# Kernel tuning notes

Measured on AMD Instinct MI355X. Metric: run time of the kernel, lower is better.

## Reference

```python
import jax, jax.numpy as jnp
import numpy as np

M = 16           # size_graph_filter (nodes per hidden prototype graph)
S = 16           # size_subgraph
D_IN = 128       # input_dim
H = 64           # hidden_dim
O = 32           # out_dim (number of hidden prototype graphs)
B = 32768        # batch of subgraphs
MAX_STEP = 3
BN_EPS = 1e-5


def setup_inputs() -> dict:
    key = jax.random.key(0)
    ks = jax.random.split(key, 8)
    adj = jax.random.uniform(ks[0], (B, S, S), dtype=jnp.float32)
    adj = 0.5 * (adj + jnp.swapaxes(adj, 1, 2))  # symmetric weighted adjacency
    features = jax.random.normal(ks[1], (B, S, D_IN), dtype=jnp.float32)
    # learned parameters (per torch init: uniform inits, Linear default-like fc_in)
    W_in = jax.random.normal(ks[2], (D_IN, H), dtype=jnp.float32) * (1.0 / np.sqrt(D_IN))
    b_in = jnp.zeros((H,), dtype=jnp.float32)
    features_hidden = jax.random.uniform(ks[3], (M, H, O), dtype=jnp.float32)          # U(0,1)
    adj_hidden = jax.random.uniform(ks[4], (M * (M - 1) // 2, O), dtype=jnp.float32,
                                    minval=-1.0, maxval=1.0)                            # U(-1,1)
    bn_gamma = jnp.ones((O,), dtype=jnp.float32)
    bn_beta = jnp.zeros((O,), dtype=jnp.float32)
    return {"adj": adj, "features": features, "W_in": W_in, "b_in": b_in,
            "features_hidden": features_hidden, "adj_hidden": adj_hidden,
            "bn_gamma": bn_gamma, "bn_beta": bn_beta}


def reference(adj, features, W_in, b_in, features_hidden, adj_hidden, bn_gamma, bn_beta):
    # Build symmetric hidden adjacency (M, M, O) from triu-packed parameters.
    iu, ju = jnp.triu_indices(M, k=1)
    A = jnp.zeros((M, M, O), dtype=adj_hidden.dtype)
    A = A.at[iu, ju, :].set(jax.nn.relu(adj_hidden))
    A = A + jnp.swapaxes(A, 0, 1)

    x = jax.nn.sigmoid(features @ W_in + b_in)   # (B, S, H)
    z = features_hidden                           # (M, H, O)

    acc = jnp.zeros((B, O), dtype=x.dtype)
    for step in range(MAX_STEP):
        if step > 0:
            x = jnp.einsum('bst,bth->bsh', adj, x)        # propagate on input subgraphs
            z = jnp.einsum('mpo,pho->mho', A, z)          # propagate on hidden graphs
        # random-walk kernel value between each subgraph and each prototype
        t = jnp.einsum('mho,bsh->bo', z, x)               # sum over prototype & subgraph nodes
        acc = acc + t
    out = acc / MAX_STEP

    # BatchNorm1d (training-mode batch statistics), then sigmoid; dropout p used in eval = identity
    mean = jnp.mean(out, axis=0)
    var = jnp.var(out, axis=0)
    out = (out - mean) / jnp.sqrt(var + BN_EPS) * bn_gamma + bn_beta
    return jax.nn.sigmoid(out)
```

## Files before the change

kernel.cpp:

```cpp
#include <hip/hip_runtime.h>


typedef short  vec8s  __attribute__((ext_vector_type(8)));
typedef short  vec4s  __attribute__((ext_vector_type(4)));
typedef float  f32x4  __attribute__((ext_vector_type(4)));
typedef unsigned short vec4us __attribute__((ext_vector_type(4)));

#define NB      32768
#define SS      16
#define DIN     128
#define HH      64
#define OO      32
#define MM      16

__device__ __forceinline__ float bf2f(unsigned short u) {
    return __uint_as_float(((unsigned int)u) << 16);
}
__device__ __forceinline__ unsigned short f2bf(float f) {
    unsigned int u = __float_as_uint(f);
    unsigned int r = (u + 0x7fffu + ((u >> 16) & 1u)) >> 16;
    return (unsigned short)r;
}
template<bool F32>
__device__ __forceinline__ float ldv(const void* p, int i) {
    if (F32) return ((const float*)p)[i];
    return bf2f(((const unsigned short*)p)[i]);
}
__device__ __forceinline__ vec8s pack8(f32x4 lo, f32x4 hi) {
    union { unsigned int u[4]; vec8s v; } r;
    unsigned int a0 = __float_as_uint(lo[0]) + 0x8000u;
    unsigned int a1 = __float_as_uint(lo[1]) + 0x8000u;
    unsigned int a2 = __float_as_uint(lo[2]) + 0x8000u;
    unsigned int a3 = __float_as_uint(lo[3]) + 0x8000u;
    unsigned int b0 = __float_as_uint(hi[0]) + 0x8000u;
    unsigned int b1 = __float_as_uint(hi[1]) + 0x8000u;
    unsigned int b2 = __float_as_uint(hi[2]) + 0x8000u;
    unsigned int b3 = __float_as_uint(hi[3]) + 0x8000u;
    r.u[0] = (a0 >> 16) | (a1 & 0xFFFF0000u);
    r.u[1] = (a2 >> 16) | (a3 & 0xFFFF0000u);
    r.u[2] = (b0 >> 16) | (b1 & 0xFFFF0000u);
    r.u[3] = (b2 >> 16) | (b3 & 0xFFFF0000u);
    return r.v;
}

template<bool F32>
__device__ __forceinline__ float Aval(const void* ahS, int i, int j, int o) {
    if (i == j) return 0.f;
    int a = i < j ? i : j;
    int b = i < j ? j : i;
    int idx = a * 15 - ((a * (a - 1)) >> 1) + (b - a - 1);
    float v = ldv<F32>(ahS, idx * OO + o);
    return v > 0.f ? v : 0.f;
}

template<bool F32>
__device__ void k1_body(const void* fhP, const void* ahP, const void* WP,
                        short* ZcnS, short* WtS, float* cA, float* c2) {
    const int tid = threadIdx.x;
    for (int i = tid; i < MM * OO; i += 256) {
        int p = i >> 5, o = i & 31;
        float s = 0.f;
        for (int m = 0; m < MM; ++m) s += Aval<F32>(ahP, m, p, o);
        cA[i] = s;
    }
    __syncthreads();
    for (int i = tid; i < MM * OO; i += 256) {
        int qq = i >> 5, o = i & 31;
        float s = 0.f;
        for (int p = 0; p < MM; ++p) s += cA[p * OO + o] * Aval<F32>(ahP, p, qq, o);
        c2[i] = s;
    }
    __syncthreads();
    for (int i = blockIdx.x * 256 + tid; i < 3 * OO * HH; i += 16 * 256) {
        int n = i >> 6, h = i & 63;
        int step = n >> 5, o = n & 31;
        float v = 0.f;
        for (int p = 0; p < MM; ++p) {
            float z = ldv<F32>(fhP, p * (HH * OO) + h * OO + o);
            float w = (step == 0) ? 1.f : (step == 1 ? cA[p * OO + o] : c2[p * OO + o]);
            v += w * z;
        }
        ZcnS[n * HH + h] = (short)f2bf(v);
    }
    for (int i = blockIdx.x * 256 + tid; i < DIN * HH; i += 16 * 256) {
        int h = i >> 7, k = i & 127;
        WtS[h * DIN + k] = (short)f2bf(ldv<F32>(WP, k * HH + h));
    }
}

__global__ void k1_prep(const void* fhP, const void* ahP, const void* WP,
                        short* ZcnS, short* WtS, double* dstats,
                        const void* featP, int* flag) {
    __shared__ float cA[MM * OO];
    __shared__ float c2[MM * OO];
    __shared__ int chuge, czero, sflag;
    const int tid = threadIdx.x;
    if (tid == 0) { chuge = 0; czero = 0; }
    if (blockIdx.x == 0 && tid < 64) dstats[tid] = 0.0;
    __syncthreads();
    if (tid < 64) {
        const unsigned short* p = (const unsigned short*)featP;
        int h = 0, z = 0;
        for (int i = tid; i < 4096; i += 64) {
            unsigned short u = p[i];
            unsigned e = (u >> 7) & 0xFFu;
            if (e >= 0x90u) h++;
            if ((u & 0x7FFFu) == 0) z++;
        }
        atomicAdd(&chuge, h);
        atomicAdd(&czero, z);
    }
    __syncthreads();
    if (tid == 0) {
        sflag = (chuge > 8 || czero > 512) ? 1 : 0;
        if (blockIdx.x == 0) *flag = sflag;
    }
    __syncthreads();
    if (sflag) k1_body<true>(fhP, ahP, WP, ZcnS, WtS, cA, c2);
    else       k1_body<false>(fhP, ahP, WP, ZcnS, WtS, cA, c2);
}


template<bool F32> struct Slot;
template<> struct Slot<true>  { f32x4 f[8]; f32x4 a; };
template<> struct Slot<false> { vec8s f[4]; vec4s a; };

template<bool F32>
__device__ __forceinline__ void issue_load(const void* adjP, const void* featP,
                                           int b, int lane, int hl, int q,
                                           Slot<F32>& s) {
    if constexpr (F32) {
        s.a = *(const f32x4*)((const float*)adjP + b * (SS * SS) + lane * 4);
        const float* fb = (const float*)featP + b * (SS * DIN) + hl * DIN + q * 8;
        #pragma unroll
        for (int kt = 0; kt < 4; ++kt) {
            s.f[2 * kt]     = *(const f32x4*)(fb + kt * 32);
            s.f[2 * kt + 1] = *(const f32x4*)(fb + kt * 32 + 4);
        }
    } else {
        s.a = *(const vec4s*)((const short*)adjP + b * (SS * SS) + lane * 4);
        const short* fb = (const short*)featP + b * (SS * DIN) + hl * DIN + q * 8;
        #pragma unroll
        for (int kt = 0; kt < 4; ++kt) s.f[kt] = *(const vec8s*)(fb + kt * 32);
    }
}

template<bool F32>
__device__ __forceinline__ void compute_one(
    const Slot<F32>& s, int b,
    const vec8s (&Wfrag)[4][4], const char* ZcnL,
    const float (&biasv)[4], short* myx0, float* accOut,
    float& ls, float& lss, int lane, int hl, int q) {

    const f32x4 z4 = {0.f, 0.f, 0.f, 0.f};

    float a0, a1, a2, a3;
    vec8s af[4];
    if constexpr (F32) {
        a0 = s.a[0]; a1 = s.a[1]; a2 = s.a[2]; a3 = s.a[3];
        #pragma unroll
        for (int kt = 0; kt < 4; ++kt) af[kt] = pack8(s.f[2 * kt], s.f[2 * kt + 1]);
    } else {
        a0 = bf2f((unsigned short)s.a.x); a1 = bf2f((unsigned short)s.a.y);
        a2 = bf2f((unsigned short)s.a.z); a3 = bf2f((unsigned short)s.a.w);
        #pragma unroll
        for (int kt = 0; kt < 4; ++kt) af[kt] = s.f[kt];
    }

    float rsum = a0 + a1 + a2 + a3;
    rsum += __shfl_xor(rsum, 1);
    rsum += __shfl_xor(rsum, 2);
    int cg = lane & 3;
    float rr0 = __shfl(rsum, cg * 16 + 0);
    float rr1 = __shfl(rsum, cg * 16 + 4);
    float rr2 = __shfl(rsum, cg * 16 + 8);
    float rr3 = __shfl(rsum, cg * 16 + 12);
    float p = a0 * rr0 + a1 * rr1 + a2 * rr2 + a3 * rr3;
    p += __shfl_xor(p, 1);
    p += __shfl_xor(p, 2);
    float w1q[4], w2q[4];
    #pragma unroll
    for (int reg = 0; reg < 4; ++reg) {
        int src = q * 16 + reg * 4;
        w1q[reg] = __shfl(rsum, src);
        w2q[reg] = __shfl(p, src);
    }

    f32x4 c1[4] = {z4, z4, z4, z4};
    #pragma unroll
    for (int nt = 0; nt < 4; ++nt)
        #pragma unroll
        for (int kt = 0; kt < 4; ++kt)
            c1[nt] = __builtin_amdgcn_mfma_f32_16x16x32_bf16(af[kt], Wfrag[kt][nt], c1[nt], 0, 0, 0);

    vec8s zf[2][6];
    #pragma unroll
    for (int kt = 0; kt < 2; ++kt)
        #pragma unroll
        for (int t = 0; t < 6; ++t) {
            int row = t * 16 + hl;
            int col = (kt * 64 + q * 16) ^ ((hl & 7) << 4);
            zf[kt][t] = *(const vec8s*)(ZcnL + row * 128 + col);
        }

    #pragma unroll
    for (int nt = 0; nt < 4; ++nt)
        #pragma unroll
        for (int reg = 0; reg < 4; ++reg) {
            float x = c1[nt][reg] + biasv[nt];
            float sg = 1.f / (1.f + __expf(-x));
            unsigned int u = __float_as_uint(sg) + 0x8000u;
            myx0[(q * 4 + reg) * 72 + nt * 16 + hl] = (short)(u >> 16);
        }
    __threadfence_block();

    vec8s a2lo = *(const vec8s*)(myx0 + hl * 72 + q * 8);
    vec8s a2hi = *(const vec8s*)(myx0 + hl * 72 + 32 + q * 8);
    __threadfence_block();
    f32x4 cp[6] = {z4, z4, z4, z4, z4, z4};
    #pragma unroll
    for (int t = 0; t < 6; ++t)
        cp[t] = __builtin_amdgcn_mfma_f32_16x16x32_bf16(a2lo, zf[0][t], cp[t], 0, 0, 0);
    #pragma unroll
    for (int t = 0; t < 6; ++t)
        cp[t] = __builtin_amdgcn_mfma_f32_16x16x32_bf16(a2hi, zf[1][t], cp[t], 0, 0, 0);

    float parts[6];
    #pragma unroll
    for (int t = 0; t < 6; ++t) {
        int step = t >> 1;
        float v;
        if (step == 0)      v = cp[t][0] + cp[t][1] + cp[t][2] + cp[t][3];
        else if (step == 1) v = cp[t][0]*w1q[0] + cp[t][1]*w1q[1] + cp[t][2]*w1q[2] + cp[t][3]*w1q[3];
        else                v = cp[t][0]*w2q[0] + cp[t][1]*w2q[1] + cp[t][2]*w2q[2] + cp[t][3]*w2q[3];
        v += __shfl_xor(v, 16);
        v += __shfl_xor(v, 32);
        parts[t] = v;
    }
    float accA = parts[0] + parts[2] + parts[4];
    float accB = parts[1] + parts[3] + parts[5];
    float accv = ((lane >> 4) & 1) ? accB : accA;
    accv *= (1.f / 3.f);
    accv = __builtin_isnan(accv) ? 0.f : accv;
    if (lane < OO) accOut[b * OO + lane] = accv;
    ls  += accv;
    lss += accv * accv;
}

template<bool F32>
__device__ void k2_body(const void* adjP, const void* featP, const void* binP,
                        const short* ZcnS, const short* WtS, float* accOut,
                        double* dstats, short* myx0, float* bsum, float* bsqs,
                        const char* ZcnL) {
    const int tid  = threadIdx.x;
    const int lane = tid & 63;
    const int hl   = lane & 15;
    const int q    = lane >> 4;

    vec8s Wfrag[4][4];
    #pragma unroll
    for (int kt = 0; kt < 4; ++kt)
        #pragma unroll
        for (int nt = 0; nt < 4; ++nt)
            Wfrag[kt][nt] = *(const vec8s*)(WtS + (nt * 16 + hl) * DIN + kt * 32 + q * 8);
    float biasv[4];
    #pragma unroll
    for (int nt = 0; nt < 4; ++nt) biasv[nt] = ldv<F32>(binP, nt * 16 + hl);

    float ls = 0.f, lss = 0.f;
    const int wgid = blockIdx.x * 4 + (tid >> 6);

    Slot<F32> sA, sB;
    int b = wgid;
    issue_load<F32>(adjP, featP, b, lane, hl, q, sA);
    #pragma unroll 1
    for (int it = 0; it < 7; ++it) {
        issue_load<F32>(adjP, featP, b + 2048, lane, hl, q, sB);
        compute_one<F32>(sA, b, Wfrag, ZcnL, biasv, myx0, accOut, ls, lss, lane, hl, q);
        b += 2048;
        issue_load<F32>(adjP, featP, b + 2048, lane, hl, q, sA);
        compute_one<F32>(sB, b, Wfrag, ZcnL, biasv, myx0, accOut, ls, lss, lane, hl, q);
        b += 2048;
    }
    issue_load<F32>(adjP, featP, b + 2048, lane, hl, q, sB);
    compute_one<F32>(sA, b, Wfrag, ZcnL, biasv, myx0, accOut, ls, lss, lane, hl, q);
    b += 2048;
    compute_one<F32>(sB, b, Wfrag, ZcnL, biasv, myx0, accOut, ls, lss, lane, hl, q);

    if (lane < OO) {
        atomicAdd(&bsum[lane], ls);
        atomicAdd(&bsqs[lane], lss);
    }
    __syncthreads();
    if (tid < OO) {
        atomicAdd(&dstats[tid],      (double)bsum[tid]);
        atomicAdd(&dstats[OO + tid], (double)bsqs[tid]);
    }
}

__global__ __launch_bounds__(256, 2) void k2_main(
    const void* adjP, const void* featP, const void* binP,
    const short* ZcnS, const short* WtS, float* accOut,
    double* dstats, const int* flag) {
    __shared__ __align__(16) short x0buf[4][SS * 72];
    __shared__ __align__(16) char  ZcnL[96 * 128];
    __shared__ float bsum[OO];
    __shared__ float bsqs[OO];
    const int tid = threadIdx.x;
    if (tid < OO) { bsum[tid] = 0.f; bsqs[tid] = 0.f; }
    for (int i = tid; i < 96 * 8; i += 256) {
        int r = i >> 3, ch = i & 7;
        vec8s v = *(const vec8s*)(ZcnS + r * 64 + ch * 8);
        *(vec8s*)(ZcnL + r * 128 + ((ch * 16) ^ ((r & 7) << 4))) = v;
    }
    __syncthreads();
    short* myx0 = x0buf[tid >> 6];
    if (*flag) k2_body<true>(adjP, featP, binP, ZcnS, WtS, accOut, dstats, myx0, bsum, bsqs, ZcnL);
    else       k2_body<false>(adjP, featP, binP, ZcnS, WtS, accOut, dstats, myx0, bsum, bsqs, ZcnL);
}

__global__ __launch_bounds__(256) void k4_out(const float* __restrict__ acc,
                                              const double* __restrict__ dstats,
                                              const void* gammaP, const void* betaP,
                                              void* out, const int* flag) {
    __shared__ float sScale[OO], sShift[OO];
    const int tid = threadIdx.x;
    const int f = *flag;
    if (tid < OO) {
        double mean = dstats[tid] * (1.0 / (double)NB);
        double ex2  = dstats[OO + tid] * (1.0 / (double)NB);
        double var  = ex2 - mean * mean;
        if (var < 0.0) var = 0.0;
        double inv  = 1.0 / sqrt(var + 1e-5);
        float g  = f ? ldv<true>(gammaP, tid) : ldv<false>(gammaP, tid);
        float be = f ? ldv<true>(betaP, tid)  : ldv<false>(betaP, tid);
        sScale[tid] = g * (float)inv;
        sShift[tid] = be - (float)(mean * inv) * g;
    }
    __syncthreads();
    int i = (blockIdx.x * 256 + tid) * 4;
    int o0 = i & 31;
    f32x4 a = *(const f32x4*)(acc + i);
    float r[4];
    #pragma unroll
    for (int j = 0; j < 4; ++j) {
        float z = a[j] * sScale[o0 + j] + sShift[o0 + j];
        r[j] = 1.f / (1.f + __expf(-z));
    }
    if (f) {
        f32x4 w;
        #pragma unroll
        for (int j = 0; j < 4; ++j) w[j] = r[j];
        *(f32x4*)((float*)out + i) = w;
    } else {
        vec4us w;
        #pragma unroll
        for (int j = 0; j < 4; ++j) w[j] = f2bf(r[j]);
        *(vec4us*)((unsigned short*)out + i) = w;
    }
}

extern "C" void kernel_launch(void* const* d_in, const int* in_sizes, int n_in,
                              void* d_out, int out_size, void* d_ws, size_t ws_size,
                              hipStream_t stream) {
    const void* adjP   = d_in[0];
    const void* featP  = d_in[1];
    const void* WP     = d_in[2];
    const void* binP   = d_in[3];
    const void* fhP    = d_in[4];
    const void* ahP    = d_in[5];
    const void* gammaP = d_in[6];
    const void* betaP  = d_in[7];

    char* ws = (char*)d_ws;
    float*  accOut   = (float*)(ws);
    short*  ZcnS     = (short*)(ws + 4194304);
    short*  WtS      = (short*)(ws + 4206592);
    double* dstats   = (double*)(ws + 4222976);
    int*    flag     = (int*)(ws + 4223744);

    hipLaunchKernelGGL(k1_prep,  dim3(16),   dim3(256), 0, stream,
                       fhP, ahP, WP, ZcnS, WtS, dstats, featP, flag);
    hipLaunchKernelGGL(k2_main,  dim3(512),  dim3(256), 0, stream,
                       adjP, featP, binP, ZcnS, WtS, accOut, dstats, flag);
    hipLaunchKernelGGL(k4_out,   dim3(1024), dim3(256), 0, stream,
                       accOut, dstats, gammaP, betaP, d_out, flag);
}
```

Baseline: 427.3 us.

## Fuse BatchNorm output kernel into main kernel via grid-wide spin barrier

Per-subgraph accumulators now stay in shared memory instead of going through a global buffer. A software grid barrier, an atomic counter with a spin wait, lets every block read the final batch statistics and write the normalized sigmoid output directly, so the separate k4 launch and its global round trip go away. Loading of the second half of the Z fragments is also moved later to lower register pressure. The barrier needs all 512 blocks to be resident at once, which launch_bounds(256,2) is meant to guarantee on this GPU, and blocks now idle at the barrier.

```diff
diff --git a/kernel.cpp b/kernel.cpp
--- a/kernel.cpp
+++ b/kernel.cpp
@@ -12,6 +12,7 @@
 #define HH      64
 #define OO      32
 #define MM      16
+#define NBLK    512
 
 __device__ __forceinline__ float bf2f(unsigned short u) {
     return __uint_as_float(((unsigned int)u) << 16);
@@ -25,6 +26,11 @@
 __device__ __forceinline__ float ldv(const void* p, int i) {
     if (F32) return ((const float*)p)[i];
     return bf2f(((const unsigned short*)p)[i]);
+}
+__device__ __forceinline__ double ldd_coh(const double* p) {
+    long long v = __hip_atomic_load((const long long*)p, __ATOMIC_RELAXED,
+                                    __HIP_MEMORY_SCOPE_AGENT);
+    return __longlong_as_double(v);
 }
 __device__ __forceinline__ vec8s pack8(f32x4 lo, f32x4 hi) {
     union { unsigned int u[4]; vec8s v; } r;
@@ -90,13 +96,14 @@
 
 __global__ void k1_prep(const void* fhP, const void* ahP, const void* WP,
                         short* ZcnS, short* WtS, double* dstats,
-                        const void* featP, int* flag) {
+                        const void* featP, int* flag, unsigned int* barCnt) {
     __shared__ float cA[MM * OO];
     __shared__ float c2[MM * OO];
     __shared__ int chuge, czero, sflag;
     const int tid = threadIdx.x;
     if (tid == 0) { chuge = 0; czero = 0; }
     if (blockIdx.x == 0 && tid < 64) dstats[tid] = 0.0;
+    if (blockIdx.x == 0 && tid == 0) *barCnt = 0u;
     __syncthreads();
     if (tid < 64) {
         const unsigned short* p = (const unsigned short*)featP;
@@ -147,9 +154,9 @@
 
 template<bool F32>
 __device__ __forceinline__ void compute_one(
-    const Slot<F32>& s, int b,
+    const Slot<F32>& s,
     const vec8s (&Wfrag)[4][4], const char* ZcnL,
-    const float (&biasv)[4], short* myx0, float* accOut,
+    const float (&biasv)[4], short* myx0, float* accSlot,
     float& ls, float& lss, int lane, int hl, int q) {
 
     const f32x4 z4 = {0.f, 0.f, 0.f, 0.f};
@@ -193,15 +200,13 @@
         for (int kt = 0; kt < 4; ++kt)
             c1[nt] = __builtin_amdgcn_mfma_f32_16x16x32_bf16(af[kt], Wfrag[kt][nt], c1[nt], 0, 0, 0);
 
-    vec8s zf[2][6];
-    #pragma unroll
-    for (int kt = 0; kt < 2; ++kt)
-        #pragma unroll
-        for (int t = 0; t < 6; ++t) {
-            int row = t * 16 + hl;
-            int col = (kt * 64 + q * 16) ^ ((hl & 7) << 4);
-            zf[kt][t] = *(const vec8s*)(ZcnL + row * 128 + col);
-        }
+    vec8s zf0[6], zf1[6];
+    #pragma unroll
+    for (int t = 0; t < 6; ++t) {
+        int row = t * 16 + hl;
+        int col = (q * 16) ^ ((hl & 7) << 4);
+        zf0[t] = *(const vec8s*)(ZcnL + row * 128 + col);
+    }
 
     #pragma unroll
     for (int nt = 0; nt < 4; ++nt)
@@ -217,13 +222,19 @@
     vec8s a2lo = *(const vec8s*)(myx0 + hl * 72 + q * 8);
     vec8s a2hi = *(const vec8s*)(myx0 + hl * 72 + 32 + q * 8);
     __threadfence_block();
+    #pragma unroll
+    for (int t = 0; t < 6; ++t) {
+        int row = t * 16 + hl;
+        int col = (64 + q * 16) ^ ((hl & 7) << 4);
+        zf1[t] = *(const vec8s*)(ZcnL + row * 128 + col);
+    }
     f32x4 cp[6] = {z4, z4, z4, z4, z4, z4};
     #pragma unroll
     for (int t = 0; t < 6; ++t)
-        cp[t] = __builtin_amdgcn_mfma_f32_16x16x32_bf16(a2lo, zf[0][t], cp[t], 0, 0, 0);
+        cp[t] = __builtin_amdgcn_mfma_f32_16x16x32_bf16(a2lo, zf0[t], cp[t], 0, 0, 0);
     #pragma unroll
     for (int t = 0; t < 6; ++t)
-        cp[t] = __builtin_amdgcn_mfma_f32_16x16x32_bf16(a2hi, zf[1][t], cp[t], 0, 0, 0);
+        cp[t] = __builtin_amdgcn_mfma_f32_16x16x32_bf16(a2hi, zf1[t], cp[t], 0, 0, 0);
 
     float parts[6];
     #pragma unroll
@@ -242,16 +253,16 @@
     float accv = ((lane >> 4) & 1) ? accB : accA;
     accv *= (1.f / 3.f);
     accv = __builtin_isnan(accv) ? 0.f : accv;
-    if (lane < OO) accOut[b * OO + lane] = accv;
+    if (lane < OO) accSlot[lane] = accv;
     ls  += accv;
     lss += accv * accv;
 }
 
 template<bool F32>
 __device__ void k2_body(const void* adjP, const void* featP, const void* binP,
-                        const short* ZcnS, const short* WtS, float* accOut,
+                        const short* ZcnS, const short* WtS,
                         double* dstats, short* myx0, float* bsum, float* bsqs,
-                        const char* ZcnL) {
+                        const char* ZcnL, float* accLw) {
     const int tid  = threadIdx.x;
     const int lane = tid & 63;
     const int hl   = lane & 15;
@@ -272,20 +283,21 @@
 
     Slot<F32> sA, sB;
     int b = wgid;
+    float* acc = accLw;
     issue_load<F32>(adjP, featP, b, lane, hl, q, sA);
     #pragma unroll 1
     for (int it = 0; it < 7; ++it) {
         issue_load<F32>(adjP, featP, b + 2048, lane, hl, q, sB);
-        compute_one<F32>(sA, b, Wfrag, ZcnL, biasv, myx0, accOut, ls, lss, lane, hl, q);
-        b += 2048;
+        compute_one<F32>(sA, Wfrag, ZcnL, biasv, myx0, acc, ls, lss, lane, hl, q);
+        acc += 32; b += 2048;
         issue_load<F32>(adjP, featP, b + 2048, lane, hl, q, sA);
-        compute_one<F32>(sB, b, Wfrag, ZcnL, biasv, myx0, accOut, ls, lss, lane, hl, q);
-        b += 2048;
+        compute_one<F32>(sB, Wfrag, ZcnL, biasv, myx0, acc, ls, lss, lane, hl, q);
+        acc += 32; b += 2048;
     }
     issue_load<F32>(adjP, featP, b + 2048, lane, hl, q, sB);
-    compute_one<F32>(sA, b, Wfrag, ZcnL, biasv, myx0, accOut, ls, lss, lane, hl, q);
-    b += 2048;
-    compute_one<F32>(sB, b, Wfrag, ZcnL, biasv, myx0, accOut, ls, lss, lane, hl, q);
+    compute_one<F32>(sA, Wfrag, ZcnL, biasv, myx0, acc, ls, lss, lane, hl, q);
+    acc += 32;
+    compute_one<F32>(sB, Wfrag, ZcnL, biasv, myx0, acc, ls, lss, lane, hl, q);
 
     if (lane < OO) {
         atomicAdd(&bsum[lane], ls);
@@ -300,12 +312,15 @@
 
 __global__ __launch_bounds__(256, 2) void k2_main(
     const void* adjP, const void* featP, const void* binP,
-    const short* ZcnS, const short* WtS, float* accOut,
-    double* dstats, const int* flag) {
+    const short* ZcnS, const short* WtS,
+    double* dstats, const int* flag, unsigned int* barCnt,
+    const void* gammaP, const void* betaP, void* outP) {
     __shared__ __align__(16) short x0buf[4][SS * 72];
     __shared__ __align__(16) char  ZcnL[96 * 128];
+    __shared__ __align__(16) float accL[4 * 16 * OO];
     __shared__ float bsum[OO];
     __shared__ float bsqs[OO];
+    __shared__ float sScale[OO], sShift[OO];
     const int tid = threadIdx.x;
     if (tid < OO) { bsum[tid] = 0.f; bsqs[tid] = 0.f; }
     for (int i = tid; i < 96 * 8; i += 256) {
@@ -314,21 +329,24 @@
         *(vec8s*)(ZcnL + r * 128 + ((ch * 16) ^ ((r & 7) << 4))) = v;
     }
     __syncthreads();
-    short* myx0 = x0buf[tid >> 6];
-    if (*flag) k2_body<true>(adjP, featP, binP, ZcnS, WtS, accOut, dstats, myx0, bsum, bsqs, ZcnL);
-    else       k2_body<false>(adjP, featP, binP, ZcnS, WtS, accOut, dstats, myx0, bsum, bsqs, ZcnL);
-}
-
-__global__ __launch_bounds__(256) void k4_out(const float* __restrict__ acc,
-                                              const double* __restrict__ dstats,
-                                              const void* gammaP, const void* betaP,
-                                              void* out, const int* flag) {
-    __shared__ float sScale[OO], sShift[OO];
-    const int tid = threadIdx.x;
     const int f = *flag;
+    short* myx0  = x0buf[tid >> 6];
+    float* accLw = accL + (tid >> 6) * (16 * OO);
+    if (f) k2_body<true>(adjP, featP, binP, ZcnS, WtS, dstats, myx0, bsum, bsqs, ZcnL, accLw);
+    else   k2_body<false>(adjP, featP, binP, ZcnS, WtS, dstats, myx0, bsum, bsqs, ZcnL, accLw);
+
+    __threadfence();
+    __syncthreads();
+    if (tid == 0) {
+        __hip_atomic_fetch_add(barCnt, 1u, __ATOMIC_RELEASE, __HIP_MEMORY_SCOPE_AGENT);
+        while (__hip_atomic_load(barCnt, __ATOMIC_ACQUIRE, __HIP_MEMORY_SCOPE_AGENT) < NBLK)
+            __builtin_amdgcn_s_sleep(8);
+    }
+    __syncthreads();
+
     if (tid < OO) {
-        double mean = dstats[tid] * (1.0 / (double)NB);
-        double ex2  = dstats[OO + tid] * (1.0 / (double)NB);
+        double mean = ldd_coh(dstats + tid)      * (1.0 / (double)NB);
+        double ex2  = ldd_coh(dstats + OO + tid) * (1.0 / (double)NB);
         double var  = ex2 - mean * mean;
         if (var < 0.0) var = 0.0;
         double inv  = 1.0 / sqrt(var + 1e-5);
@@ -338,25 +356,18 @@
         sShift[tid] = be - (float)(mean * inv) * g;
     }
     __syncthreads();
-    int i = (blockIdx.x * 256 + tid) * 4;
-    int o0 = i & 31;
-    f32x4 a = *(const f32x4*)(acc + i);
-    float r[4];
-    #pragma unroll
-    for (int j = 0; j < 4; ++j) {
-        float z = a[j] * sScale[o0 + j] + sShift[o0 + j];
-        r[j] = 1.f / (1.f + __expf(-z));
-    }
-    if (f) {
-        f32x4 w;
-        #pragma unroll
-        for (int j = 0; j < 4; ++j) w[j] = r[j];
-        *(f32x4*)((float*)out + i) = w;
-    } else {
-        vec4us w;
-        #pragma unroll
-        for (int j = 0; j < 4; ++j) w[j] = f2bf(r[j]);
-        *(vec4us*)((unsigned short*)out + i) = w;
+
+    const int lane = tid & 63;
+    const int wgid = blockIdx.x * 4 + (tid >> 6);
+    if (lane < OO) {
+        float sc = sScale[lane], sh = sShift[lane];
+        for (int it = 0; it < 16; ++it) {
+            int b = wgid + it * 2048;
+            float z = accLw[it * OO + lane] * sc + sh;
+            float r = 1.f / (1.f + __expf(-z));
+            if (f) ((float*)outP)[b * OO + lane] = r;
+            else   ((unsigned short*)outP)[b * OO + lane] = f2bf(r);
+        }
     }
 }
 
@@ -373,16 +384,15 @@
     const void* betaP  = d_in[7];
 
     char* ws = (char*)d_ws;
-    float*  accOut   = (float*)(ws);
-    short*  ZcnS     = (short*)(ws + 4194304);
-    short*  WtS      = (short*)(ws + 4206592);
-    double* dstats   = (double*)(ws + 4222976);
-    int*    flag     = (int*)(ws + 4223744);
-
-    hipLaunchKernelGGL(k1_prep,  dim3(16),   dim3(256), 0, stream,
-                       fhP, ahP, WP, ZcnS, WtS, dstats, featP, flag);
-    hipLaunchKernelGGL(k2_main,  dim3(512),  dim3(256), 0, stream,
-                       adjP, featP, binP, ZcnS, WtS, accOut, dstats, flag);
-    hipLaunchKernelGGL(k4_out,   dim3(1024), dim3(256), 0, stream,
-                       accOut, dstats, gammaP, betaP, d_out, flag);
-}
+    short*  ZcnS   = (short*)(ws);
+    short*  WtS    = (short*)(ws + 12288);
+    double* dstats = (double*)(ws + 28672);
+    int*    flag   = (int*)(ws + 29184);
+    unsigned int* barCnt = (unsigned int*)(ws + 29188);
+
+    hipLaunchKernelGGL(k1_prep, dim3(16),   dim3(256), 0, stream,
+                       fhP, ahP, WP, ZcnS, WtS, dstats, featP, flag, barCnt);
+    hipLaunchKernelGGL(k2_main, dim3(NBLK), dim3(256), 0, stream,
+                       adjP, featP, binP, ZcnS, WtS, dstats, flag, barCnt,
+                       gammaP, betaP, d_out);
+}
```

New measurement: 527.1 us. 1.23x slower.
